# Performance work log

Hardware: AMD Instinct MI355X
Metric: run time of the kernel (lower is better)

## Reference

```python
import jax, jax.numpy as jnp
import numpy as np

N_NODES = 100000
N_EDGES = 1600000
D_FEAT = 64
D_OUT = 64


def setup_inputs() -> dict:
    key = jax.random.key(0)
    ks = jax.random.split(key, 8)
    return {
        "feat": jax.random.normal(ks[0], (N_NODES, D_FEAT), dtype=jnp.float32),
        "emb": jax.random.normal(ks[1], (N_NODES, D_OUT), dtype=jnp.float32),
        "W1": jax.random.normal(ks[2], (D_OUT, D_FEAT), dtype=jnp.float32) * 0.1,
        "b1": jax.random.normal(ks[3], (D_OUT,), dtype=jnp.float32) * 0.1,
        "W2": jax.random.normal(ks[4], (D_OUT, D_OUT), dtype=jnp.float32) * 0.1,
        "b2": jax.random.normal(ks[5], (D_OUT,), dtype=jnp.float32) * 0.1,
        "edge_src": jax.random.randint(ks[6], (N_EDGES,), 0, N_NODES, dtype=jnp.int32),
        "edge_dst": jax.random.randint(ks[7], (N_EDGES,), 0, N_NODES, dtype=jnp.int32),
    }


def reference(feat, emb, W1, b1, W2, b2, edge_src, edge_dst):
    # n2v: per-node neighbor embedding sum (vectorized gather + segment-sum)
    n_nodes = feat.shape[0]
    nbr_sum = jax.ops.segment_sum(emb[edge_src], edge_dst, num_segments=n_nodes)  # [N, D_OUT]
    new_emb = jax.nn.relu(feat @ W1.T + b1 + nbr_sum @ W2.T + b2)  # [N, D_OUT]
    # g2v: graph embedding = sum of node embeddings
    graph_emb = new_emb.sum(axis=0)  # [D_OUT]
    return graph_emb
```

## Files before the change

### kernel.cpp

```cpp
#include <hip/hip_runtime.h>

#define N_NODES 100000
#define N_EDGES 1600000
#define D 64
#define CAP 32
#define OVF_CAP 8192
#define N_TILES 1563
#define NR 8
#define SLICE_EDGES 2048
#define N_SLICES 782
#define R1_BLOCKS 64
#define R1_ROWS 25
#define ASTRIDE 136

#define NB2 782
#define BCAP2 2560
#define EPB 8192
#define P1_BLOCKS 196
#define CVT_BLOCKS 64

typedef int    vint4  __attribute__((ext_vector_type(4)));
typedef short  s16x4  __attribute__((ext_vector_type(4)));
typedef short  s16x8  __attribute__((ext_vector_type(8)));
typedef float  f32x2  __attribute__((ext_vector_type(2)));
typedef float  f32x4  __attribute__((ext_vector_type(4)));
typedef __bf16 bf16x8 __attribute__((ext_vector_type(8)));

__device__ inline short f2bf(float f) {
    unsigned u = __builtin_bit_cast(unsigned, f);
    u += 0x7fffu + ((u >> 16) & 1u);
    return (short)(u >> 16);
}
__device__ inline s16x4 f2bf4(float4 v) {
    s16x4 r; r.x = f2bf(v.x); r.y = f2bf(v.y); r.z = f2bf(v.z); r.w = f2bf(v.w);
    return r;
}
__device__ inline float bf2f(short s) {
    return __builtin_bit_cast(float, ((unsigned)(unsigned short)s) << 16);
}

#define WS_SLOTS_OFF  401408
#define WS_ACC_OFF    13201408
#define WS_ACC16_OFF  13201408
#define WS_OVFC_OFF   38801408
#define WS_OVF_OFF    38801424
#define WS_PART_OFF   38867200
#define WS_PART2_OFF  39267328
#define WS_EMB8_OFF   39283712
#define WS_NEEDED     (WS_PART2_OFF + R1_BLOCKS * 64 * 4)
#define WS_NEEDED16   (WS_EMB8_OFF + N_NODES * D * 2)

__global__ __launch_bounds__(512) void part_kernel(
    const int* __restrict__ edge_src, const int* __restrict__ edge_dst,
    int* __restrict__ bcnt, int* __restrict__ bkt,
    int* __restrict__ ovf_cnt, int2* __restrict__ ovf,
    const float* __restrict__ emb, unsigned* __restrict__ emb8) {
    const int tid = threadIdx.x;
    if (blockIdx.x >= P1_BLOCKS) {
        const float4* e4 = (const float4*)emb;
        const unsigned t0 = (blockIdx.x - P1_BLOCKS) * 512 + tid;
        for (unsigned j = t0; j < (unsigned)(N_NODES * D / 4);
             j += CVT_BLOCKS * 512) {
            float4 v = e4[j];
            int w = 0;
            w = __builtin_amdgcn_cvt_pk_fp8_f32(v.x, v.y, w, false);
            w = __builtin_amdgcn_cvt_pk_fp8_f32(v.z, v.w, w, true);
            emb8[j] = (unsigned)w;
        }
        return;
    }

    __shared__ int stage[EPB];
    __shared__ unsigned short bid[EPB];
    __shared__ int scA[1024];
    __shared__ int scB[1024];
    __shared__ int hist[NB2];
    int* const cur   = scB;
    int* const gbase = scA;

    const int e0 = blockIdx.x * EPB;
    for (int i = tid; i < NB2; i += 512) hist[i] = 0;
    __syncthreads();

    int ss[16], dd[16];
#pragma unroll
    for (int i = 0; i < 16; ++i) {
        const int e = e0 + i * 512 + tid;
        if (e < N_EDGES) { ss[i] = edge_src[e]; dd[i] = edge_dst[e]; }
        else             { ss[i] = 0; dd[i] = -1; }
    }

#pragma unroll
    for (int i = 0; i < 16; ++i)
        if (dd[i] >= 0) atomicAdd(&hist[dd[i] >> 7], 1);
    __syncthreads();

    scA[tid]       = (tid < NB2) ? hist[tid] : 0;
    scA[tid + 512] = 0;
    if (tid + 512 < NB2) scA[tid + 512] = hist[tid + 512];
    __syncthreads();
    {
        int* sA = scA;
        int* sB = scB;
        for (int off = 1; off < 1024; off <<= 1) {
            const int i1 = tid + 512;
            const int v0 = sA[tid] + ((tid >= off) ? sA[tid - off] : 0);
            const int v1 = sA[i1] + sA[i1 - off];
            sB[tid] = v0; sB[i1] = v1;
            __syncthreads();
            int* t = sA; sA = sB; sB = t;
        }
    }
    const int tot = scA[NB2 - 1];
    for (int i = tid; i < NB2; i += 512) cur[i] = scA[i] - hist[i];
    __syncthreads();

#pragma unroll
    for (int i = 0; i < 16; ++i) {
        if (dd[i] >= 0) {
            const int b = dd[i] >> 7;
            const int pos = atomicAdd(&cur[b], 1);
            stage[pos] = (ss[i] << 7) | (dd[i] & 127);
            bid[pos] = (unsigned short)b;
        }
    }
    for (int i = tid; i < NB2; i += 512)
        gbase[i] = atomicAdd(&bcnt[i], hist[i]);
    __syncthreads();

    for (int j = tid; j < tot; j += 512) {
        const int pk = stage[j];
        const int b  = bid[j];
        const int gpos = gbase[b] + (j - (cur[b] - hist[b]));
        if (gpos < BCAP2) {
            bkt[b * BCAP2 + gpos] = pk;
        } else {
            int oj = atomicAdd(ovf_cnt, 1);
            if (oj < OVF_CAP) ovf[oj] = make_int2(pk >> 7, (b << 7) | (pk & 127));
        }
    }
}

__global__ __launch_bounds__(512) void fill2_kernel(
    const int* __restrict__ bcnt, const int* __restrict__ bkt,
    int* __restrict__ cnt, int* __restrict__ slots,
    int* __restrict__ ovf_cnt, int2* __restrict__ ovf) {
    __shared__ int lcnt[128];
    const int b = blockIdx.x;
    const int tid = threadIdx.x;
    if (tid < 128) lcnt[tid] = 0;
    __syncthreads();
    int n = bcnt[b];
    if (n > BCAP2) n = BCAP2;
    for (int i = tid; i < n; i += 512) {
        const int pk = bkt[b * BCAP2 + i];
        const int dl = pk & 127;
        const int pos = atomicAdd(&lcnt[dl], 1);
        const int v = (b << 7) | dl;
        if (pos < CAP) {
            slots[v * CAP + pos] = pk >> 7;
        } else {
            int j = atomicAdd(ovf_cnt, 1);
            if (j < OVF_CAP) ovf[j] = make_int2(pk >> 7, v);
        }
    }
    __syncthreads();
    if (tid < 128) {
        const int v = (b << 7) | tid;
        if (v < N_NODES) cnt[v] = lcnt[tid];
    }
}

__global__ __launch_bounds__(256) void gather8_kernel(
    const unsigned* __restrict__ emb8, const int* __restrict__ cnt,
    const int* __restrict__ slots, short* __restrict__ acc16) {
    const int lane = threadIdx.x & 63;
    const int wave = threadIdx.x >> 6;
    const int v = blockIdx.x * 4 + wave;
    const int q = lane >> 4;
    const int c = lane & 15;
    int deg = cnt[v];
    if (deg > CAP) deg = CAP;
    const int si = slots[v * CAP + (lane & (CAP - 1))];

    float4 sum = make_float4(0.f, 0.f, 0.f, 0.f);
#pragma unroll
    for (int e = 0; e < CAP; e += 8) {
        const int i0 = e + q, i1 = e + 4 + q;
        const int s0 = __shfl(si, i0);
        const int s1 = __shfl(si, i1);
        unsigned x0 = 0u, x1 = 0u;
        if (i0 < deg) x0 = emb8[(unsigned)s0 * 16 + c];
        if (i1 < deg) x1 = emb8[(unsigned)s1 * 16 + c];
        const f32x2 a0 = __builtin_amdgcn_cvt_pk_f32_fp8((int)x0, false);
        const f32x2 a1 = __builtin_amdgcn_cvt_pk_f32_fp8((int)x0, true);
        const f32x2 b0 = __builtin_amdgcn_cvt_pk_f32_fp8((int)x1, false);
        const f32x2 b1 = __builtin_amdgcn_cvt_pk_f32_fp8((int)x1, true);
        sum.x += a0.x + b0.x;
        sum.y += a0.y + b0.y;
        sum.z += a1.x + b1.x;
        sum.w += a1.y + b1.y;
    }
#pragma unroll
    for (int off = 16; off < 64; off <<= 1) {
        sum.x += __shfl_xor(sum.x, off);
        sum.y += __shfl_xor(sum.y, off);
        sum.z += __shfl_xor(sum.z, off);
        sum.w += __shfl_xor(sum.w, off);
    }
    if (q == 0) {
        *(s16x4*)&acc16[v * D + c * 4] = f2bf4(sum);
    }
}

__global__ __launch_bounds__(64) void ovf2_kernel(
    const float* __restrict__ emb, const int* __restrict__ ovf_cnt,
    const int2* __restrict__ ovf, short* __restrict__ acc16) {
    int n = *ovf_cnt;
    if (n > OVF_CAP) n = OVF_CAP;
    const int l = threadIdx.x;
    for (int i = 0; i < n; ++i) {
        const int2 e = ovf[i];
        const float a = bf2f(acc16[e.y * D + l]) + emb[e.x * D + l];
        acc16[e.y * D + l] = f2bf(a);
    }
}

__global__ __launch_bounds__(256) void fill_kernel(
    const int* __restrict__ edge_src, const int* __restrict__ edge_dst,
    int* __restrict__ cnt, int* __restrict__ slots,
    int* __restrict__ ovf_cnt, int2* __restrict__ ovf) {
    const int r = blockIdx.x & (NR - 1);
    if (r == 7) return;
    const int slice = blockIdx.x >> 3;
    const int base_e = slice * SLICE_EDGES + threadIdx.x * 8;
    if (base_e >= N_EDGES) return;
    const vint4* s4 = (const vint4*)(edge_src + base_e);
    const vint4* d4 = (const vint4*)(edge_dst + base_e);
    vint4 a0 = __builtin_nontemporal_load(s4);
    vint4 a1 = __builtin_nontemporal_load(s4 + 1);
    vint4 b0 = __builtin_nontemporal_load(d4);
    vint4 b1 = __builtin_nontemporal_load(d4 + 1);
    int ss[8] = {a0.x, a0.y, a0.z, a0.w, a1.x, a1.y, a1.z, a1.w};
    int dd[8] = {b0.x, b0.y, b0.z, b0.w, b1.x, b1.y, b1.z, b1.w};
    int pos[8];
#pragma unroll
    for (int i = 0; i < 8; ++i) {
        pos[i] = ((dd[i] >> 14) == r) ? atomicAdd(&cnt[dd[i]], 1) : -1;
    }
#pragma unroll
    for (int i = 0; i < 8; ++i) {
        if (pos[i] >= 0 && pos[i] < CAP) slots[dd[i] * CAP + pos[i]] = ss[i];
    }
#pragma unroll
    for (int i = 0; i < 8; ++i) {
        if (pos[i] >= CAP) {
            int j = atomicAdd(ovf_cnt, 1);
            if (j < OVF_CAP) ovf[j] = make_int2(ss[i], dd[i]);
        }
    }
}

__global__ __launch_bounds__(256) void gather_kernel(
    const float* __restrict__ emb, const int* __restrict__ cnt,
    const int* __restrict__ slots, float* __restrict__ acc) {
    const int lane = threadIdx.x & 63;
    const int wave = threadIdx.x >> 6;
    const int v = blockIdx.x * 4 + wave;
    const int q  = lane >> 4;
    const int c4 = lane & 15;
    int deg = cnt[v];
    if (deg > CAP) deg = CAP;
    const int si = slots[v * CAP + (lane & (CAP - 1))];
    const float4* emb4 = (const float4*)emb;

    float4 sum = make_float4(0.f, 0.f, 0.f, 0.f);
    for (int e = 0; e < deg; e += 4) {
        const int idx = e + q;
        const int s = __shfl(si, idx & (CAP - 1));
        if (idx < deg) {
            float4 a = emb4[s * 16 + c4];
            sum.x += a.x; sum.y += a.y; sum.z += a.z; sum.w += a.w;
        }
    }
#pragma unroll
    for (int off = 16; off < 64; off <<= 1) {
        sum.x += __shfl_xor(sum.x, off);
        sum.y += __shfl_xor(sum.y, off);
        sum.z += __shfl_xor(sum.z, off);
        sum.w += __shfl_xor(sum.w, off);
    }
    if (q == 0) {
        ((float4*)acc)[v * 16 + c4] = sum;
    }
}

__global__ __launch_bounds__(256) void ovf_kernel(
    const float* __restrict__ emb, const int* __restrict__ ovf_cnt,
    const int2* __restrict__ ovf, float* __restrict__ acc) {
    int n = *ovf_cnt;
    if (n > OVF_CAP) n = OVF_CAP;
    const int lane = threadIdx.x & 63;
    const int wv = (blockIdx.x * 256 + threadIdx.x) >> 6;
    const int nwaves = (gridDim.x * 256) >> 6;
    for (int i = wv; i < n; i += nwaves) {
        int2 e = ovf[i];
        unsafeAtomicAdd(&acc[e.y * D + lane], emb[e.x * D + lane]);
    }
}

__global__ __launch_bounds__(256) void scatter_kernel(
    const float* __restrict__ emb,
    const int* __restrict__ edge_src, const int* __restrict__ edge_dst,
    float* __restrict__ acc) {
    int gid = blockIdx.x * 256 + threadIdx.x;
    int e = gid >> 6;
    int c = gid & 63;
    unsafeAtomicAdd(&acc[edge_dst[e] * D + c], emb[edge_src[e] * D + c]);
}

__global__ __launch_bounds__(256) void final_mixed_kernel(
    const float* __restrict__ feat, const short* __restrict__ acc16,
    const float* __restrict__ W1, const float* __restrict__ b1,
    const float* __restrict__ W2, const float* __restrict__ b2,
    float* __restrict__ partials) {
    __shared__ short A_s[64 * ASTRIDE];
    __shared__ short W_s[64 * ASTRIDE];
    __shared__ float red[4][64];

    const int tid  = threadIdx.x;
    const int lane = tid & 63;
    const int wave = tid >> 6;
    const int quad = lane >> 4;
    const int col  = lane & 15;
    const int node0 = blockIdx.x * 64;

    float bias[4];
#pragma unroll
    for (int nb = 0; nb < 4; ++nb) {
        const int o = nb * 16 + col;
        bias[nb] = b1[o] + b2[o];
    }

    {
        const float4* W1v = (const float4*)W1;
        const float4* W2v = (const float4*)W2;
#pragma unroll
        for (int i = 0; i < 4; ++i) {
            const int flat = tid + i * 256;
            const int row = flat >> 4, c4 = flat & 15;
            *(s16x4*)&W_s[row * ASTRIDE + c4 * 4]      = f2bf4(W1v[flat]);
            *(s16x4*)&W_s[row * ASTRIDE + 64 + c4 * 4] = f2bf4(W2v[flat]);
        }
    }

    {
        const float4* fv = (const float4*)feat;
#pragma unroll
        for (int i = 0; i < 4; ++i) {
            const int flat = tid + i * 256;
            const int row = flat >> 4, c4 = flat & 15;
            const int node = node0 + row;
            float4 f = make_float4(0.f, 0.f, 0.f, 0.f);
            if (node < N_NODES) f = fv[(size_t)node * 16 + c4];
            *(s16x4*)&A_s[row * ASTRIDE + c4 * 4] = f2bf4(f);
        }
    }
    {
#pragma unroll
        for (int i = 0; i < 2; ++i) {
            const int flat = tid + i * 256;
            const int row = flat >> 3, c = flat & 7;
            const int node = node0 + row;
            s16x8 pk = {0, 0, 0, 0, 0, 0, 0, 0};
            if (node < N_NODES) pk = *(const s16x8*)&acc16[node * D + c * 8];
            *(s16x8*)&A_s[row * ASTRIDE + 64 + c * 8] = pk;
        }
    }
    __syncthreads();

    bf16x8 Bf[4][4];
#pragma unroll
    for (int nb = 0; nb < 4; ++nb)
#pragma unroll
        for (int ks = 0; ks < 4; ++ks)
            Bf[nb][ks] = __builtin_bit_cast(bf16x8,
                *(const s16x8*)&W_s[(nb * 16 + col) * ASTRIDE + ks * 32 + quad * 8]);

    f32x4 C[4];
#pragma unroll
    for (int nb = 0; nb < 4; ++nb) C[nb] = (f32x4){0.f, 0.f, 0.f, 0.f};
#pragma unroll
    for (int ks = 0; ks < 4; ++ks) {
        const bf16x8 Af = __builtin_bit_cast(bf16x8,
            *(const s16x8*)&A_s[(wave * 16 + col) * ASTRIDE + ks * 32 + quad * 8]);
#pragma unroll
        for (int nb = 0; nb < 4; ++nb)
            C[nb] = __builtin_amdgcn_mfma_f32_16x16x32_bf16(Af, Bf[nb][ks],
                                                            C[nb], 0, 0, 0);
    }

    float sums[4] = {0.f, 0.f, 0.f, 0.f};
#pragma unroll
    for (int nb = 0; nb < 4; ++nb) {
#pragma unroll
        for (int reg = 0; reg < 4; ++reg) {
            const int node = node0 + wave * 16 + quad * 4 + reg;
            float u = C[nb][reg] + bias[nb];
            u = (u > 0.f) ? u : 0.f;
            if (node < N_NODES) sums[nb] += u;
        }
        sums[nb] += __shfl_xor(sums[nb], 16);
        sums[nb] += __shfl_xor(sums[nb], 32);
        if (lane < 16) red[wave][nb * 16 + lane] = sums[nb];
    }
    __syncthreads();
    if (tid < 64) {
        partials[blockIdx.x * 64 + tid] =
            red[0][tid] + red[1][tid] + red[2][tid] + red[3][tid];
    }
}

__global__ __launch_bounds__(256) void final_kernel(
    const float* __restrict__ feat, const float* __restrict__ acc,
    const float* __restrict__ W1, const float* __restrict__ b1,
    const float* __restrict__ W2, const float* __restrict__ b2,
    float* __restrict__ partials) {
    __shared__ short A_s[64 * ASTRIDE];
    __shared__ short W_s[64 * ASTRIDE];
    __shared__ float red[4][64];

    const int tid  = threadIdx.x;
    const int lane = tid & 63;
    const int wave = tid >> 6;
    const int quad = lane >> 4;
    const int col  = lane & 15;
    const int node0 = blockIdx.x * 64;

    float bias[4];
#pragma unroll
    for (int nb = 0; nb < 4; ++nb) {
        const int o = nb * 16 + col;
        bias[nb] = b1[o] + b2[o];
    }

    {
        const float4* W1v = (const float4*)W1;
        const float4* W2v = (const float4*)W2;
#pragma unroll
        for (int i = 0; i < 4; ++i) {
            const int flat = tid + i * 256;
            const int row = flat >> 4, c4 = flat & 15;
            *(s16x4*)&W_s[row * ASTRIDE + c4 * 4]      = f2bf4(W1v[flat]);
            *(s16x4*)&W_s[row * ASTRIDE + 64 + c4 * 4] = f2bf4(W2v[flat]);
        }
    }

    {
        const float4* fv = (const float4*)feat;
        const float4* av = (const float4*)acc;
#pragma unroll
        for (int i = 0; i < 4; ++i) {
            const int flat = tid + i * 256;
            const int row = flat >> 4, c4 = flat & 15;
            const int node = node0 + row;
            float4 f = make_float4(0.f, 0.f, 0.f, 0.f);
            float4 n = make_float4(0.f, 0.f, 0.f, 0.f);
            if (node < N_NODES) {
                f = fv[(size_t)node * 16 + c4];
                n = av[(size_t)node * 16 + c4];
            }
            *(s16x4*)&A_s[row * ASTRIDE + c4 * 4]      = f2bf4(f);
            *(s16x4*)&A_s[row * ASTRIDE + 64 + c4 * 4] = f2bf4(n);
        }
    }
    __syncthreads();

    bf16x8 Bf[4][4];
#pragma unroll
    for (int nb = 0; nb < 4; ++nb)
#pragma unroll
        for (int ks = 0; ks < 4; ++ks)
            Bf[nb][ks] = __builtin_bit_cast(bf16x8,
                *(const s16x8*)&W_s[(nb * 16 + col) * ASTRIDE + ks * 32 + quad * 8]);

    f32x4 C[4];
#pragma unroll
    for (int nb = 0; nb < 4; ++nb) C[nb] = (f32x4){0.f, 0.f, 0.f, 0.f};
#pragma unroll
    for (int ks = 0; ks < 4; ++ks) {
        const bf16x8 Af = __builtin_bit_cast(bf16x8,
            *(const s16x8*)&A_s[(wave * 16 + col) * ASTRIDE + ks * 32 + quad * 8]);
#pragma unroll
        for (int nb = 0; nb < 4; ++nb)
            C[nb] = __builtin_amdgcn_mfma_f32_16x16x32_bf16(Af, Bf[nb][ks],
                                                            C[nb], 0, 0, 0);
    }

    float sums[4] = {0.f, 0.f, 0.f, 0.f};
#pragma unroll
    for (int nb = 0; nb < 4; ++nb) {
#pragma unroll
        for (int reg = 0; reg < 4; ++reg) {
            const int node = node0 + wave * 16 + quad * 4 + reg;
            float u = C[nb][reg] + bias[nb];
            u = (u > 0.f) ? u : 0.f;
            if (node < N_NODES) sums[nb] += u;
        }
        sums[nb] += __shfl_xor(sums[nb], 16);
        sums[nb] += __shfl_xor(sums[nb], 32);
        if (lane < 16) red[wave][nb * 16 + lane] = sums[nb];
    }
    __syncthreads();
    if (tid < 64) {
        partials[blockIdx.x * 64 + tid] =
            red[0][tid] + red[1][tid] + red[2][tid] + red[3][tid];
    }
}

__global__ __launch_bounds__(256) void reduce1_kernel(
    const float* __restrict__ partials, float* __restrict__ part2) {
    __shared__ float red[4][64];
    const int col = threadIdx.x & 63;
    const int seg = threadIdx.x >> 6;
    const int r0 = blockIdx.x * R1_ROWS;
    int r1 = r0 + R1_ROWS;
    if (r1 > N_TILES) r1 = N_TILES;
    float s = 0.f;
    for (int r = r0 + seg; r < r1; r += 4) s += partials[r * 64 + col];
    red[seg][col] = s;
    __syncthreads();
    if (seg == 0) {
        part2[blockIdx.x * 64 + col] =
            red[0][col] + red[1][col] + red[2][col] + red[3][col];
    }
}

__global__ __launch_bounds__(256) void reduce2_kernel(
    const float* __restrict__ part2, float* __restrict__ out) {
    __shared__ float red[4][64];
    const int col = threadIdx.x & 63;
    const int seg = threadIdx.x >> 6;
    float s = 0.f;
    for (int r = seg; r < R1_BLOCKS; r += 4) s += part2[r * 64 + col];
    red[seg][col] = s;
    __syncthreads();
    if (seg == 0) {
        out[col] = red[0][col] + red[1][col] + red[2][col] + red[3][col];
    }
}

extern "C" void kernel_launch(void* const* d_in, const int* in_sizes, int n_in,
                              void* d_out, int out_size, void* d_ws, size_t ws_size,
                              hipStream_t stream) {
    const float* feat = (const float*)d_in[0];
    const float* emb  = (const float*)d_in[1];
    const float* W1   = (const float*)d_in[2];
    const float* b1   = (const float*)d_in[3];
    const float* W2   = (const float*)d_in[4];
    const float* b2   = (const float*)d_in[5];
    const int* edge_src = (const int*)d_in[6];
    const int* edge_dst = (const int*)d_in[7];
    float* out = (float*)d_out;
    char* ws = (char*)d_ws;

    if (ws_size >= (size_t)WS_NEEDED16) {
        int*      cnt      = (int*)ws;
        int*      slots    = (int*)(ws + WS_SLOTS_OFF);
        short*    acc16    = (short*)(ws + WS_ACC16_OFF);
        int*      bkt      = (int*)(ws + WS_ACC16_OFF);
        int*      ovf_cnt  = (int*)(ws + WS_OVFC_OFF);
        int2*     ovf      = (int2*)(ws + WS_OVF_OFF);
        float*    partials = (float*)(ws + WS_PART_OFF);
        int*      bcnt     = (int*)(ws + WS_PART_OFF);
        float*    part2    = (float*)(ws + WS_PART2_OFF);
        unsigned* emb8     = (unsigned*)(ws + WS_EMB8_OFF);

        (void)hipMemsetAsync(ovf_cnt, 0, sizeof(int), stream);
        (void)hipMemsetAsync(bcnt, 0, NB2 * sizeof(int), stream);

        part_kernel<<<P1_BLOCKS + CVT_BLOCKS, 512, 0, stream>>>(
            edge_src, edge_dst, bcnt, bkt, ovf_cnt, ovf, emb, emb8);
        fill2_kernel<<<NB2, 512, 0, stream>>>(bcnt, bkt, cnt, slots,
                                              ovf_cnt, ovf);
        gather8_kernel<<<N_NODES / 4, 256, 0, stream>>>(emb8, cnt, slots, acc16);
        ovf2_kernel<<<1, 64, 0, stream>>>(emb, ovf_cnt, ovf, acc16);

        final_mixed_kernel<<<N_TILES, 256, 0, stream>>>(feat, acc16, W1, b1,
                                                        W2, b2, partials);
        reduce1_kernel<<<R1_BLOCKS, 256, 0, stream>>>(partials, part2);
        reduce2_kernel<<<1, 256, 0, stream>>>(part2, out);
    } else if (ws_size >= (size_t)WS_NEEDED) {
        int*   cnt      = (int*)ws;
        int*   slots    = (int*)(ws + WS_SLOTS_OFF);
        float* acc      = (float*)(ws + WS_ACC_OFF);
        int*   ovf_cnt  = (int*)(ws + WS_OVFC_OFF);
        int2*  ovf      = (int2*)(ws + WS_OVF_OFF);
        float* partials = (float*)(ws + WS_PART_OFF);
        float* part2    = (float*)(ws + WS_PART2_OFF);

        (void)hipMemsetAsync(cnt, 0, N_NODES * sizeof(int), stream);
        (void)hipMemsetAsync(ovf_cnt, 0, sizeof(int), stream);

        fill_kernel<<<NR * N_SLICES, 256, 0, stream>>>(edge_src, edge_dst,
                                                       cnt, slots, ovf_cnt, ovf);
        gather_kernel<<<N_NODES / 4, 256, 0, stream>>>(emb, cnt, slots, acc);
        ovf_kernel<<<16, 256, 0, stream>>>(emb, ovf_cnt, ovf, acc);

        final_kernel<<<N_TILES, 256, 0, stream>>>(feat, acc, W1, b1, W2, b2,
                                                  partials);
        reduce1_kernel<<<R1_BLOCKS, 256, 0, stream>>>(partials, part2);
        reduce2_kernel<<<1, 256, 0, stream>>>(part2, out);
    } else {
        float* acc = (float*)ws;
        (void)hipMemsetAsync(acc, 0, (size_t)N_NODES * D * sizeof(float), stream);
        scatter_kernel<<<(N_EDGES * 64) / 256, 256, 0, stream>>>(emb, edge_src,
                                                                 edge_dst, acc);
        float* partials = (float*)(ws + (size_t)N_NODES * D * sizeof(float));
        float* part2    = partials + (size_t)N_TILES * 64;
        final_kernel<<<N_TILES, 256, 0, stream>>>(feat, acc, W1, b1, W2, b2,
                                                  partials);
        reduce1_kernel<<<R1_BLOCKS, 256, 0, stream>>>(partials, part2);
        reduce2_kernel<<<1, 256, 0, stream>>>(part2, out);
    }
}
```

Before: 191.7 us.

## Fuse bucket fill and neighbor gather into one kernel using LDS slot lists

Merges fill2 and gather8 into a single kernel. Each block now builds its 128 nodes' neighbor lists in shared memory and gathers FP8 embeddings straight from them, so the cnt/slots arrays are no longer written to and read back from global memory and one launch disappears. The gather loop now runs only up to each node's degree instead of a fixed unrolled CAP. The tradeoff is less parallelism in the gather: there are 782 blocks of 8 waves, each wave serially handling 16 nodes, instead of 25000 small blocks. The extra 16KB of LDS per block may also limit occupancy.

```diff
diff --git a/kernel.cpp b/kernel.cpp
--- a/kernel.cpp
+++ b/kernel.cpp
@@ -141,75 +141,72 @@
     }
 }
 
-__global__ __launch_bounds__(512) void fill2_kernel(
+__global__ __launch_bounds__(512) void fillgather_kernel(
     const int* __restrict__ bcnt, const int* __restrict__ bkt,
-    int* __restrict__ cnt, int* __restrict__ slots,
-    int* __restrict__ ovf_cnt, int2* __restrict__ ovf) {
+    const unsigned* __restrict__ emb8,
+    int* __restrict__ ovf_cnt, int2* __restrict__ ovf,
+    short* __restrict__ acc16) {
     __shared__ int lcnt[128];
+    __shared__ int lslots[128 * CAP];
     const int b = blockIdx.x;
     const int tid = threadIdx.x;
     if (tid < 128) lcnt[tid] = 0;
     __syncthreads();
+
     int n = bcnt[b];
     if (n > BCAP2) n = BCAP2;
     for (int i = tid; i < n; i += 512) {
         const int pk = bkt[b * BCAP2 + i];
         const int dl = pk & 127;
         const int pos = atomicAdd(&lcnt[dl], 1);
-        const int v = (b << 7) | dl;
         if (pos < CAP) {
-            slots[v * CAP + pos] = pk >> 7;
+            lslots[dl * CAP + pos] = pk >> 7;
         } else {
             int j = atomicAdd(ovf_cnt, 1);
-            if (j < OVF_CAP) ovf[j] = make_int2(pk >> 7, v);
-        }
-    }
-    __syncthreads();
-    if (tid < 128) {
-        const int v = (b << 7) | tid;
-        if (v < N_NODES) cnt[v] = lcnt[tid];
-    }
-}
-
-__global__ __launch_bounds__(256) void gather8_kernel(
-    const unsigned* __restrict__ emb8, const int* __restrict__ cnt,
-    const int* __restrict__ slots, short* __restrict__ acc16) {
-    const int lane = threadIdx.x & 63;
-    const int wave = threadIdx.x >> 6;
-    const int v = blockIdx.x * 4 + wave;
+            if (j < OVF_CAP) ovf[j] = make_int2(pk >> 7, (b << 7) | dl);
+        }
+    }
+    __syncthreads();
+
+    const int lane = tid & 63;
+    const int wave = tid >> 6;
     const int q = lane >> 4;
     const int c = lane & 15;
-    int deg = cnt[v];
-    if (deg > CAP) deg = CAP;
-    const int si = slots[v * CAP + (lane & (CAP - 1))];
-
-    float4 sum = make_float4(0.f, 0.f, 0.f, 0.f);
-#pragma unroll
-    for (int e = 0; e < CAP; e += 8) {
-        const int i0 = e + q, i1 = e + 4 + q;
-        const int s0 = __shfl(si, i0);
-        const int s1 = __shfl(si, i1);
-        unsigned x0 = 0u, x1 = 0u;
-        if (i0 < deg) x0 = emb8[(unsigned)s0 * 16 + c];
-        if (i1 < deg) x1 = emb8[(unsigned)s1 * 16 + c];
-        const f32x2 a0 = __builtin_amdgcn_cvt_pk_f32_fp8((int)x0, false);
-        const f32x2 a1 = __builtin_amdgcn_cvt_pk_f32_fp8((int)x0, true);
-        const f32x2 b0 = __builtin_amdgcn_cvt_pk_f32_fp8((int)x1, false);
-        const f32x2 b1 = __builtin_amdgcn_cvt_pk_f32_fp8((int)x1, true);
-        sum.x += a0.x + b0.x;
-        sum.y += a0.y + b0.y;
-        sum.z += a1.x + b1.x;
-        sum.w += a1.y + b1.y;
-    }
-#pragma unroll
-    for (int off = 16; off < 64; off <<= 1) {
-        sum.x += __shfl_xor(sum.x, off);
-        sum.y += __shfl_xor(sum.y, off);
-        sum.z += __shfl_xor(sum.z, off);
-        sum.w += __shfl_xor(sum.w, off);
-    }
-    if (q == 0) {
-        *(s16x4*)&acc16[v * D + c * 4] = f2bf4(sum);
+#pragma unroll 1
+    for (int t = 0; t < 16; ++t) {
+        const int dl = wave * 16 + t;
+        const int v = (b << 7) | dl;
+        int deg = lcnt[dl];
+        if (deg > CAP) deg = CAP;
+        const int si = lslots[dl * CAP + (lane & (CAP - 1))];
+
+        float4 sum = make_float4(0.f, 0.f, 0.f, 0.f);
+        for (int e = 0; e < deg; e += 8) {
+            const int i0 = e + q, i1 = e + 4 + q;
+            const int s0 = __shfl(si, i0 & (CAP - 1));
+            const int s1 = __shfl(si, i1 & (CAP - 1));
+            unsigned x0 = 0u, x1 = 0u;
+            if (i0 < deg) x0 = emb8[(unsigned)s0 * 16 + c];
+            if (i1 < deg) x1 = emb8[(unsigned)s1 * 16 + c];
+            const f32x2 a0 = __builtin_amdgcn_cvt_pk_f32_fp8((int)x0, false);
+            const f32x2 a1 = __builtin_amdgcn_cvt_pk_f32_fp8((int)x0, true);
+            const f32x2 b0 = __builtin_amdgcn_cvt_pk_f32_fp8((int)x1, false);
+            const f32x2 b1 = __builtin_amdgcn_cvt_pk_f32_fp8((int)x1, true);
+            sum.x += a0.x + b0.x;
+            sum.y += a0.y + b0.y;
+            sum.z += a1.x + b1.x;
+            sum.w += a1.y + b1.y;
+        }
+#pragma unroll
+        for (int off = 16; off < 64; off <<= 1) {
+            sum.x += __shfl_xor(sum.x, off);
+            sum.y += __shfl_xor(sum.y, off);
+            sum.z += __shfl_xor(sum.z, off);
+            sum.w += __shfl_xor(sum.w, off);
+        }
+        if (q == 0 && v < N_NODES) {
+            *(s16x4*)&acc16[v * D + c * 4] = f2bf4(sum);
+        }
     }
 }
 
@@ -565,10 +562,8 @@
     char* ws = (char*)d_ws;
 
     if (ws_size >= (size_t)WS_NEEDED16) {
-        int*      cnt      = (int*)ws;
-        int*      slots    = (int*)(ws + WS_SLOTS_OFF);
+        int*      bkt      = (int*)ws;
         short*    acc16    = (short*)(ws + WS_ACC16_OFF);
-        int*      bkt      = (int*)(ws + WS_ACC16_OFF);
         int*      ovf_cnt  = (int*)(ws + WS_OVFC_OFF);
         int2*     ovf      = (int2*)(ws + WS_OVF_OFF);
         float*    partials = (float*)(ws + WS_PART_OFF);
@@ -581,9 +576,8 @@
 
         part_kernel<<<P1_BLOCKS + CVT_BLOCKS, 512, 0, stream>>>(
             edge_src, edge_dst, bcnt, bkt, ovf_cnt, ovf, emb, emb8);
-        fill2_kernel<<<NB2, 512, 0, stream>>>(bcnt, bkt, cnt, slots,
-                                              ovf_cnt, ovf);
-        gather8_kernel<<<N_NODES / 4, 256, 0, stream>>>(emb8, cnt, slots, acc16);
+        fillgather_kernel<<<NB2, 512, 0, stream>>>(bcnt, bkt, emb8,
+                                                   ovf_cnt, ovf, acc16);
         ovf2_kernel<<<1, 64, 0, stream>>>(emb, ovf_cnt, ovf, acc16);
 
         final_mixed_kernel<<<N_TILES, 256, 0, stream>>>(feat, acc16, W1, b1,
```

Measured after the change: 181.8 us. 5.2% less time.
